# Kernel optimization log

Measured on AMD Instinct MI355X. Metric: run time of the kernel, lower is better.

## Reference

```python
import jax, jax.numpy as jnp
import numpy as np


def setup_inputs() -> dict:
    key = jax.random.key(0)
    gramBatch = jax.random.normal(key, (8, 8, 1024, 16, 16), dtype=jnp.float32)
    return {"gramBatch": gramBatch, "patchPerRow": 32}


def reference(gramBatch, patchPerRow):
    # Parallel (parralelMode=True) path of GramDistMap.forward.
    B, C, N, D1, D2 = gramBatch.shape
    g = gramBatch.reshape(B, C, N, D1 * D2)            # [B,C,N,D]
    # gramNorm = sqrt(sum((g*g)^2)) = sqrt(sum(g^4))
    g2 = g * g
    norm = jnp.sqrt(jnp.sum(g2 * g2, axis=-1))         # [B,C,N]
    # sum_d (g_i - g_j)^2 = ||g_i||^2 + ||g_j||^2 - 2 g_i . g_j,
    # computed without materializing the [B,C,N,N,D] broadcast tensor.
    sq = jnp.sum(g2, axis=-1)                          # [B,C,N]
    dots = jnp.einsum('bcnd,bcmd->bcnm', g, g)         # [B,C,N,N]
    dist2 = sq[..., :, None] + sq[..., None, :] - 2.0 * dots
    distMat = dist2 / (norm[..., :, None] * norm[..., None, :])
    return distMat.mean(axis=1)                        # [B,N,N]
```

## Files before the change

kernel.cpp:

```cpp
#include <hip/hip_runtime.h>
#include <stdint.h>

#define NB 8
#define NC 8
#define NN 1024
#define ND 256
#define KK 2048
#define BM 128
#define BN 128
#define BKK 64
#define NT (KK / BKK)

typedef float f32x4 __attribute__((ext_vector_type(4)));
typedef short bf16x8 __attribute__((ext_vector_type(8)));

__device__ __forceinline__ unsigned short f2bf(float x) {
  union { float f; uint32_t u; } a; a.f = x;
  uint32_t u = a.u;
  return (unsigned short)((u + 0x7FFFu + ((u >> 16) & 1u)) >> 16);
}

__device__ __forceinline__ void gload16(const void* g, void* l) {
  __builtin_amdgcn_global_load_lds(
      (__attribute__((address_space(1))) uint32_t*)g,
      (__attribute__((address_space(3))) uint32_t*)l, 16, 0, 0);
}

__global__ __launch_bounds__(256) void prep_kernel(
    const float* __restrict__ g, unsigned short* __restrict__ ghat,
    float* __restrict__ uv) {
  int wid = blockIdx.x * 4 + (threadIdx.x >> 6);
  int lane = threadIdx.x & 63;
#pragma unroll
  for (int j = 0; j < 4; ++j) {
    int rowid = wid * 4 + j;
    int n = rowid & (NN - 1);
    int bc = rowid >> 10;
    int c = bc & (NC - 1);
    int b = bc >> 3;
    const float* row = g + (size_t)rowid * ND;
    f32x4 v = *(const f32x4*)(row + lane * 4);
    float s2 = 0.f, s4 = 0.f;
#pragma unroll
    for (int q = 0; q < 4; ++q) { float x2 = v[q] * v[q]; s2 += x2; s4 += x2 * x2; }
#pragma unroll
    for (int off = 32; off; off >>= 1) {
      s2 += __shfl_xor(s2, off);
      s4 += __shfl_xor(s4, off);
    }
    float rn = rsqrtf(s4);
    ushort4 o;
    o.x = f2bf(v[0] * rn); o.y = f2bf(v[1] * rn);
    o.z = f2bf(v[2] * rn); o.w = f2bf(v[3] * rn);
    size_t gh = ((size_t)(b * NN + n)) * KK + (size_t)c * ND + lane * 4;
    *(ushort4*)(ghat + gh) = o;
    if (lane == 0) {
      size_t uvo = ((size_t)(b * NN + n)) * 16;
      uv[uvo + c] = s2 * rn;
      uv[uvo + 8 + c] = rn;
    }
  }
}

__device__ __forceinline__ void stage_tile(const unsigned short* __restrict__ gsrc,
                                           unsigned short* lds, int k0, int tid) {
  int r = tid >> 3;
  int s = tid & 7;
  int sg = s ^ (r & 7);
#pragma unroll
  for (int i = 0; i < 4; ++i) {
    int rr = i * 32 + r;
    gload16(gsrc + (size_t)rr * KK + k0 + sg * 8, lds + rr * BKK + s * 8);
  }
}

__global__ __launch_bounds__(256) void gram_gemm_kernel(
    const unsigned short* __restrict__ ghat, const float* __restrict__ uv,
    float* __restrict__ out) {
  __shared__ union {
    struct { unsigned short A[2][BM * BKK]; unsigned short Bt[2][BN * BKK]; } s;
    struct { float R[128][16]; float Cc[128][16]; } e;
  } sm;

  int bid = blockIdx.x;
  int logical = (bid & 7) * (NB * 64 / 8) + (bid >> 3);
  int b = logical >> 6;
  int t6 = logical & 63;
  int row0 = (t6 >> 3) * BM;
  int col0 = (t6 & 7) * BN;
  int tid = threadIdx.x;
  int lane = tid & 63;
  int wave = tid >> 6;
  int wr = (wave >> 1) * 64;
  int wc = (wave & 1) * 64;

  const unsigned short* gA = ghat + (size_t)(b * NN + row0) * KK;
  const unsigned short* gB = ghat + (size_t)(b * NN + col0) * KK;

  f32x4 acc[4][4];
#pragma unroll
  for (int i = 0; i < 4; ++i)
#pragma unroll
    for (int j = 0; j < 4; ++j)
      acc[i][j] = f32x4{0.f, 0.f, 0.f, 0.f};

  int rsel = lane & 15;
  int khalf = lane >> 4;

  stage_tile(gA, sm.s.A[0], 0, tid);
  stage_tile(gB, sm.s.Bt[0], 0, tid);
  __syncthreads();

  int cur = 0;
  for (int t = 0; t < NT; ++t) {
    if (t + 1 < NT) {
      stage_tile(gA, sm.s.A[cur ^ 1], (t + 1) * BKK, tid);
      stage_tile(gB, sm.s.Bt[cur ^ 1], (t + 1) * BKK, tid);
    }
#pragma unroll
    for (int kk = 0; kk < 2; ++kk) {
      bf16x8 af[4], bfb[4];
#pragma unroll
      for (int i = 0; i < 4; ++i) {
        int rr = wr + i * 16 + rsel;
        int slot = (kk * 4 + khalf) ^ (rr & 7);
        af[i] = *(const bf16x8*)&sm.s.A[cur][rr * BKK + slot * 8];
      }
#pragma unroll
      for (int j = 0; j < 4; ++j) {
        int rr = wc + j * 16 + rsel;
        int slot = (kk * 4 + khalf) ^ (rr & 7);
        bfb[j] = *(const bf16x8*)&sm.s.Bt[cur][rr * BKK + slot * 8];
      }
#pragma unroll
      for (int i = 0; i < 4; ++i)
#pragma unroll
        for (int j = 0; j < 4; ++j)
          acc[i][j] = __builtin_amdgcn_mfma_f32_16x16x32_bf16(af[i], bfb[j], acc[i][j], 0, 0, 0);
    }
    __syncthreads();
    cur ^= 1;
  }

  {
    const f32x4* srcR = (const f32x4*)(uv + (size_t)(b * NN + row0) * 16);
    const f32x4* srcC = (const f32x4*)(uv + (size_t)(b * NN + col0) * 16);
    f32x4* dR = (f32x4*)&sm.e.R[0][0];
    f32x4* dC = (f32x4*)&sm.e.Cc[0][0];
#pragma unroll
    for (int i = 0; i < 2; ++i) {
      dR[tid + i * 256] = srcR[tid + i * 256];
      dC[tid + i * 256] = srcC[tid + i * 256];
    }
  }
  __syncthreads();

  int lr = (lane >> 4) * 4;
  int lc = lane & 15;
#pragma unroll
  for (int j = 0; j < 4; ++j) {
    int cl = wc + j * 16 + lc;
    f32x4 uc0 = *(const f32x4*)&sm.e.Cc[cl][0];
    f32x4 uc1 = *(const f32x4*)&sm.e.Cc[cl][4];
    f32x4 vc0 = *(const f32x4*)&sm.e.Cc[cl][8];
    f32x4 vc1 = *(const f32x4*)&sm.e.Cc[cl][12];
#pragma unroll
    for (int i = 0; i < 4; ++i) {
#pragma unroll
      for (int q = 0; q < 4; ++q) {
        int rl = wr + i * 16 + lr + q;
        f32x4 r0 = *(const f32x4*)&sm.e.R[rl][0];
        f32x4 r1 = *(const f32x4*)&sm.e.R[rl][4];
        f32x4 r2 = *(const f32x4*)&sm.e.R[rl][8];
        f32x4 r3 = *(const f32x4*)&sm.e.R[rl][12];
        float fr = r0[0]*vc0[0]+r0[1]*vc0[1]+r0[2]*vc0[2]+r0[3]*vc0[3]
                 + r1[0]*vc1[0]+r1[1]*vc1[1]+r1[2]*vc1[2]+r1[3]*vc1[3]
                 + r2[0]*uc0[0]+r2[1]*uc0[1]+r2[2]*uc0[2]+r2[3]*uc0[3]
                 + r3[0]*uc1[0]+r3[1]*uc1[1]+r3[2]*uc1[2]+r3[3]*uc1[3];
        float val = 0.125f * fr - 0.25f * acc[i][j][q];
        out[((size_t)(b * NN + row0 + rl)) * NN + (size_t)(col0 + cl)] = val;
      }
    }
  }
}

extern "C" void kernel_launch(void* const* d_in, const int* in_sizes, int n_in,
                              void* d_out, int out_size, void* d_ws, size_t ws_size,
                              hipStream_t stream) {
  const float* g = (const float*)d_in[0];
  unsigned short* ghat = (unsigned short*)d_ws;
  float* uv = (float*)((char*)d_ws + (size_t)NB * NN * KK * 2);
  float* outp = (float*)d_out;

  prep_kernel<<<NB * NC * NN / 16, 256, 0, stream>>>(g, ghat, uv);
  gram_gemm_kernel<<<NB * 64, 256, 0, stream>>>(ghat, uv, outp);
}
```

Baseline: 227.1 us.

## Halve GEMM column tile, drop LDS double buffering, flatten u/v layout

The column tile shrinks from 128 to 64, so the GEMM launches 1024 blocks instead of 512, giving more parallelism across the CUs. The double-buffered LDS staging is replaced by a single buffer with sync-load-compute-sync per K step, which cuts LDS use and may allow more blocks per CU. The cost is that global loads no longer overlap MFMA work inside a block. The per-row u/v norm terms move from an interleaved [row][16] layout to flat per-channel arrays, which makes the epilogue gather strided scalar loads.

```diff
diff --git a/kernel.cpp b/kernel.cpp
--- a/kernel.cpp
+++ b/kernel.cpp
@@ -7,7 +7,7 @@
 #define ND 256
 #define KK 2048
 #define BM 128
-#define BN 128
+#define BN 64
 #define BKK 64
 #define NT (KK / BKK)
 
@@ -28,7 +28,7 @@
 
 __global__ __launch_bounds__(256) void prep_kernel(
     const float* __restrict__ g, unsigned short* __restrict__ ghat,
-    float* __restrict__ uv) {
+    float* __restrict__ uFlat, float* __restrict__ vFlat) {
   int wid = blockIdx.x * 4 + (threadIdx.x >> 6);
   int lane = threadIdx.x & 63;
 #pragma unroll
@@ -55,102 +55,98 @@
     size_t gh = ((size_t)(b * NN + n)) * KK + (size_t)c * ND + lane * 4;
     *(ushort4*)(ghat + gh) = o;
     if (lane == 0) {
-      size_t uvo = ((size_t)(b * NN + n)) * 16;
-      uv[uvo + c] = s2 * rn;
-      uv[uvo + 8 + c] = rn;
+      uFlat[rowid] = s2 * rn;
+      vFlat[rowid] = rn;
     }
   }
 }
 
-__device__ __forceinline__ void stage_tile(const unsigned short* __restrict__ gsrc,
-                                           unsigned short* lds, int k0, int tid) {
-  int r = tid >> 3;
-  int s = tid & 7;
-  int sg = s ^ (r & 7);
-#pragma unroll
-  for (int i = 0; i < 4; ++i) {
-    int rr = i * 32 + r;
-    gload16(gsrc + (size_t)rr * KK + k0 + sg * 8, lds + rr * BKK + s * 8);
-  }
-}
-
 __global__ __launch_bounds__(256) void gram_gemm_kernel(
-    const unsigned short* __restrict__ ghat, const float* __restrict__ uv,
+    const unsigned short* __restrict__ ghat,
+    const float* __restrict__ uFlat, const float* __restrict__ vFlat,
     float* __restrict__ out) {
   __shared__ union {
-    struct { unsigned short A[2][BM * BKK]; unsigned short Bt[2][BN * BKK]; } s;
-    struct { float R[128][16]; float Cc[128][16]; } e;
+    struct { unsigned short A[BM * BKK]; unsigned short Bt[BN * BKK]; } s;
+    struct { float R[128][16]; float Cc[64][16]; } e;
   } sm;
 
   int bid = blockIdx.x;
-  int logical = (bid & 7) * (NB * 64 / 8) + (bid >> 3);
-  int b = logical >> 6;
-  int t6 = logical & 63;
-  int row0 = (t6 >> 3) * BM;
-  int col0 = (t6 & 7) * BN;
+  int logical = (bid & 7) * 128 + (bid >> 3);
+  int b = logical >> 7;
+  int t7 = logical & 127;
+  int row0 = (t7 >> 4) * BM;
+  int col0 = (t7 & 15) * BN;
   int tid = threadIdx.x;
   int lane = tid & 63;
   int wave = tid >> 6;
   int wr = (wave >> 1) * 64;
-  int wc = (wave & 1) * 64;
+  int wc = (wave & 1) * 32;
 
   const unsigned short* gA = ghat + (size_t)(b * NN + row0) * KK;
   const unsigned short* gB = ghat + (size_t)(b * NN + col0) * KK;
 
-  f32x4 acc[4][4];
+  f32x4 acc[4][2];
 #pragma unroll
   for (int i = 0; i < 4; ++i)
 #pragma unroll
-    for (int j = 0; j < 4; ++j)
+    for (int j = 0; j < 2; ++j)
       acc[i][j] = f32x4{0.f, 0.f, 0.f, 0.f};
 
   int rsel = lane & 15;
   int khalf = lane >> 4;
+  int r8 = tid >> 3;
+  int s8 = tid & 7;
 
-  stage_tile(gA, sm.s.A[0], 0, tid);
-  stage_tile(gB, sm.s.Bt[0], 0, tid);
-  __syncthreads();
-
-  int cur = 0;
   for (int t = 0; t < NT; ++t) {
-    if (t + 1 < NT) {
-      stage_tile(gA, sm.s.A[cur ^ 1], (t + 1) * BKK, tid);
-      stage_tile(gB, sm.s.Bt[cur ^ 1], (t + 1) * BKK, tid);
+    int k0 = t * BKK;
+#pragma unroll
+    for (int i = 0; i < 4; ++i) {
+      int rr = i * 32 + r8;
+      int sg = s8 ^ (rr & 7);
+      gload16(gA + (size_t)rr * KK + k0 + sg * 8, sm.s.A + rr * BKK + s8 * 8);
     }
 #pragma unroll
+    for (int i = 0; i < 2; ++i) {
+      int rr = i * 32 + r8;
+      int sg = s8 ^ (rr & 7);
+      gload16(gB + (size_t)rr * KK + k0 + sg * 8, sm.s.Bt + rr * BKK + s8 * 8);
+    }
+    __syncthreads();
+#pragma unroll
     for (int kk = 0; kk < 2; ++kk) {
-      bf16x8 af[4], bfb[4];
+      bf16x8 af[4], bfb[2];
 #pragma unroll
       for (int i = 0; i < 4; ++i) {
         int rr = wr + i * 16 + rsel;
         int slot = (kk * 4 + khalf) ^ (rr & 7);
-        af[i] = *(const bf16x8*)&sm.s.A[cur][rr * BKK + slot * 8];
+        af[i] = *(const bf16x8*)&sm.s.A[rr * BKK + slot * 8];
       }
 #pragma unroll
-      for (int j = 0; j < 4; ++j) {
+      for (int j = 0; j < 2; ++j) {
         int rr = wc + j * 16 + rsel;
         int slot = (kk * 4 + khalf) ^ (rr & 7);
-        bfb[j] = *(const bf16x8*)&sm.s.Bt[cur][rr * BKK + slot * 8];
+        bfb[j] = *(const bf16x8*)&sm.s.Bt[rr * BKK + slot * 8];
       }
 #pragma unroll
       for (int i = 0; i < 4; ++i)
 #pragma unroll
-        for (int j = 0; j < 4; ++j)
+        for (int j = 0; j < 2; ++j)
           acc[i][j] = __builtin_amdgcn_mfma_f32_16x16x32_bf16(af[i], bfb[j], acc[i][j], 0, 0, 0);
     }
     __syncthreads();
-    cur ^= 1;
   }
 
   {
-    const f32x4* srcR = (const f32x4*)(uv + (size_t)(b * NN + row0) * 16);
-    const f32x4* srcC = (const f32x4*)(uv + (size_t)(b * NN + col0) * 16);
-    f32x4* dR = (f32x4*)&sm.e.R[0][0];
-    f32x4* dC = (f32x4*)&sm.e.Cc[0][0];
+    int rl = tid >> 1;
+    int half = tid & 1;
+    const float* src = half ? vFlat : uFlat;
 #pragma unroll
-    for (int i = 0; i < 2; ++i) {
-      dR[tid + i * 256] = srcR[tid + i * 256];
-      dC[tid + i * 256] = srcC[tid + i * 256];
+    for (int c = 0; c < 8; ++c)
+      sm.e.R[rl][half * 8 + c] = src[(size_t)(b * NC + c) * NN + row0 + rl];
+    if (rl < 64) {
+#pragma unroll
+      for (int c = 0; c < 8; ++c)
+        sm.e.Cc[rl][half * 8 + c] = src[(size_t)(b * NC + c) * NN + col0 + rl];
     }
   }
   __syncthreads();
@@ -158,7 +154,7 @@
   int lr = (lane >> 4) * 4;
   int lc = lane & 15;
 #pragma unroll
-  for (int j = 0; j < 4; ++j) {
+  for (int j = 0; j < 2; ++j) {
     int cl = wc + j * 16 + lc;
     f32x4 uc0 = *(const f32x4*)&sm.e.Cc[cl][0];
     f32x4 uc1 = *(const f32x4*)&sm.e.Cc[cl][4];
@@ -189,9 +185,10 @@
                               hipStream_t stream) {
   const float* g = (const float*)d_in[0];
   unsigned short* ghat = (unsigned short*)d_ws;
-  float* uv = (float*)((char*)d_ws + (size_t)NB * NN * KK * 2);
+  float* uFlat = (float*)((char*)d_ws + (size_t)NB * NN * KK * 2);
+  float* vFlat = uFlat + (size_t)NB * NC * NN;
   float* outp = (float*)d_out;
 
-  prep_kernel<<<NB * NC * NN / 16, 256, 0, stream>>>(g, ghat, uv);
-  gram_gemm_kernel<<<NB * 64, 256, 0, stream>>>(ghat, uv, outp);
+  prep_kernel<<<NB * NC * NN / 16, 256, 0, stream>>>(g, ghat, uFlat, vFlat);
+  gram_gemm_kernel<<<NB * 128 * 8 / 8 , 256, 0, stream>>>(ghat, uFlat, vFlat, outp);
 }
```

Result: faster. 210.9 us (-7.1%).
